# Optimization experiments

Hardware: AMD Instinct MI355X
Metric: run time of the kernel (lower is better)

Reference implementation:

```python
import jax, jax.numpy as jnp
import numpy as np

N = 100000
IN_DIM = 128
OUT_DIM = 128
E = 320000


def setup_inputs() -> dict:
    key = jax.random.key(0)
    ks = jax.random.split(key, 12)
    x = jax.random.normal(ks[0], (N, IN_DIM), dtype=jnp.float32)
    src0 = jax.random.randint(ks[1], (E,), 0, N)
    dst0 = jax.random.randint(ks[2], (E,), 0, N)
    src1 = jax.random.randint(ks[3], (E,), 0, N)
    dst1 = jax.random.randint(ks[4], (E,), 0, N)
    s = 1.0 / np.sqrt(IN_DIM)
    W0 = jax.random.uniform(ks[5], (IN_DIM, OUT_DIM), minval=-s, maxval=s)
    b0 = jax.random.uniform(ks[6], (OUT_DIM,), minval=-s, maxval=s)
    W1 = jax.random.uniform(ks[7], (IN_DIM, OUT_DIM), minval=-s, maxval=s)
    b1 = jax.random.uniform(ks[8], (OUT_DIM,), minval=-s, maxval=s)
    sa = 1.0 / np.sqrt(2 * OUT_DIM)
    a0 = jax.random.uniform(ks[9], (2 * OUT_DIM,), minval=-sa, maxval=sa)
    a1 = jax.random.uniform(ks[10], (2 * OUT_DIM,), minval=-sa, maxval=sa)
    return {"x": x, "src0": src0, "dst0": dst0, "src1": src1, "dst1": dst1,
            "W0": W0, "b0": b0, "a0": a0, "W1": W1, "b1": b1, "a1": a1}


def _rel_gat(x, src, dst, W, b, a):
    # wh = Linear(in_dim, out_dim)(x)  -> [N, D]
    wh = x @ W + b
    D = wh.shape[1]
    # e = leaky_relu(a^T [wh_src || wh_dst]) ; split a instead of concat on edges
    e = jax.nn.leaky_relu(wh[src] @ a[:D] + wh[dst] @ a[D:])  # [E]
    # segment softmax over incoming edges of each dst node
    m = jax.ops.segment_max(e, dst, num_segments=N)
    ex = jnp.exp(e - m[dst])
    denom = jax.ops.segment_sum(ex, dst, num_segments=N)
    alpha = ex / denom[dst]  # [E]
    # weighted scatter-sum of src features (zero for isolated dst nodes)
    return jax.ops.segment_sum(alpha[:, None] * wh[src], dst, num_segments=N)


def reference(x, src0, dst0, src1, dst1, W0, b0, a0, W1, b1, a1):
    h0 = _rel_gat(x, src0, dst0, W0, b0, a0)
    h1 = _rel_gat(x, src1, dst1, W1, b1, a1)
    # cross-relation 'sum' reducer
    return h0 + h1
```

## Files before the change

### kernel.cpp

```cpp
#include <hip/hip_runtime.h>
#include <hip/hip_bf16.h>


typedef __bf16 bf16x8 __attribute__((ext_vector_type(8)));
typedef float f32x4 __attribute__((ext_vector_type(4)));

#define DIM 128

__global__ __launch_bounds__(256) void gemm_wh_kernel(
    const float* __restrict__ x,
    const float* __restrict__ W0, const float* __restrict__ W1,
    const float* __restrict__ b0, const float* __restrict__ b1,
    const float* __restrict__ a0, const float* __restrict__ a1,
    const int* __restrict__ dst0, const int* __restrict__ dst1,
    unsigned* __restrict__ deg,
    __bf16* __restrict__ wh, float* __restrict__ s_src,
    float* __restrict__ s_dst, int N, int E)
{
    __shared__ __align__(16) __bf16 lW[2 * 128 * 136];
    const int tid = threadIdx.x;

    {
        const int gid = blockIdx.x * 256 + tid;
        if (gid < E) {
            atomicAdd(deg + dst0[gid], 1u);
            atomicAdd(deg + N + dst1[gid], 1u);
        }
    }

    for (int i = tid; i < 2 * 128 * 128; i += 256) {
        const int r = i >> 14, idx = i & 16383;
        const int k = idx >> 7, n = idx & 127;
        const float* W = r ? W1 : W0;
        lW[r * 17408 + n * 136 + k] = (__bf16)W[idx];
    }
    __syncthreads();

    const int lane = tid & 63;
    const int wave = tid >> 6;
    const int quad = lane >> 4;
    const int mr   = lane & 15;

    const long row0 = (long)blockIdx.x * 64 + wave * 16;
    long arow = row0 + mr;
    if (arow >= N) arow = N - 1;
    const f32x4* xr = (const f32x4*)(x + arow * DIM);

    f32x4 zero = {0.f, 0.f, 0.f, 0.f};
    f32x4 acc[2][8];
#pragma unroll
    for (int r = 0; r < 2; ++r)
#pragma unroll
        for (int t = 0; t < 8; ++t) acc[r][t] = zero;

#pragma unroll
    for (int ko = 0; ko < 128; ko += 32) {
        const int jb = (ko >> 2) + quad * 2;
        f32x4 lo = xr[jb], hi = xr[jb + 1];
        bf16x8 afrag = { (__bf16)lo.x, (__bf16)lo.y, (__bf16)lo.z, (__bf16)lo.w,
                         (__bf16)hi.x, (__bf16)hi.y, (__bf16)hi.z, (__bf16)hi.w };
#pragma unroll
        for (int r = 0; r < 2; ++r)
#pragma unroll
            for (int ct = 0; ct < 8; ++ct) {
                bf16x8 bfrag = *(const bf16x8*)(&lW[r * 17408 + (ct * 16 + mr) * 136 + ko + quad * 8]);
                acc[r][ct] = __builtin_amdgcn_mfma_f32_16x16x32_bf16(afrag, bfrag, acc[r][ct], 0, 0, 0);
            }
    }
    __syncthreads();

    __bf16* Cst = lW;
#pragma unroll
    for (int r = 0; r < 2; ++r) {
        const float* bias = r ? b1 : b0;
        const float* a    = r ? a1 : a0;
        float psr[4] = {0.f, 0.f, 0.f, 0.f};
        float pdr[4] = {0.f, 0.f, 0.f, 0.f};
#pragma unroll
        for (int ct = 0; ct < 8; ++ct) {
            const int c = ct * 16 + mr;
            const float bn = bias[c];
            const float asc = a[c], adc = a[DIM + c];
#pragma unroll
            for (int rr = 0; rr < 4; ++rr) {
                const float wv = acc[r][ct][rr] + bn;
                Cst[(wave * 16 + quad * 4 + rr) * 136 + c] = (__bf16)wv;
                psr[rr] += asc * wv;
                pdr[rr] += adc * wv;
            }
        }
#pragma unroll
        for (int off = 1; off < 16; off <<= 1) {
#pragma unroll
            for (int rr = 0; rr < 4; ++rr) {
                psr[rr] += __shfl_xor(psr[rr], off);
                pdr[rr] += __shfl_xor(pdr[rr], off);
            }
        }
        if (mr == 0) {
#pragma unroll
            for (int rr = 0; rr < 4; ++rr) {
                const long orow = row0 + quad * 4 + rr;
                if (orow < N) {
                    s_src[(size_t)r * N + orow] = psr[rr];
                    s_dst[(size_t)r * N + orow] = pdr[rr];
                }
            }
        }
        __syncthreads();
#pragma unroll
        for (int i = 0; i < 4; ++i) {
            const int chunk = tid + 256 * i;
            const int row = chunk >> 4, c8 = chunk & 15;
            bf16x8 v = *(const bf16x8*)&Cst[row * 136 + c8 * 8];
            const long grow = (long)blockIdx.x * 64 + row;
            if (grow < N)
                *(bf16x8*)(wh + ((size_t)r * N + grow) * DIM + c8 * 8) = v;
        }
        __syncthreads();
    }
}

__global__ __launch_bounds__(256) void scanA_kernel(
    const unsigned* __restrict__ deg, unsigned* __restrict__ tmp,
    unsigned* __restrict__ bsum, int n)
{
    __shared__ unsigned s[256];
    const int t = threadIdx.x;
    const int i = blockIdx.x * 256 + t;
    unsigned v = (i < n) ? deg[i] : 0u;
    s[t] = v;
    __syncthreads();
#pragma unroll
    for (int off = 1; off < 256; off <<= 1) {
        unsigned add = (t >= off) ? s[t - off] : 0u;
        __syncthreads();
        s[t] += add;
        __syncthreads();
    }
    if (i < n) tmp[i] = s[t] - v;
    if (t == 255) bsum[blockIdx.x] = s[t];
}

__global__ __launch_bounds__(256) void scanB_kernel(
    const unsigned* __restrict__ bsum, unsigned* __restrict__ bsumEx, int nb)
{
    __shared__ unsigned s[256];
    const int t = threadIdx.x;
    unsigned loc[4], sum = 0u;
#pragma unroll
    for (int k = 0; k < 4; ++k) {
        int idx = t * 4 + k;
        loc[k] = (idx < nb) ? bsum[idx] : 0u;
        sum += loc[k];
    }
    s[t] = sum;
    __syncthreads();
#pragma unroll
    for (int off = 1; off < 256; off <<= 1) {
        unsigned add = (t >= off) ? s[t - off] : 0u;
        __syncthreads();
        s[t] += add;
        __syncthreads();
    }
    unsigned run = s[t] - sum;
#pragma unroll
    for (int k = 0; k < 4; ++k) {
        int idx = t * 4 + k;
        if (idx < nb) bsumEx[idx] = run;
        run += loc[k];
    }
}

__global__ __launch_bounds__(256) void scanC_kernel(
    const unsigned* __restrict__ tmp, const unsigned* __restrict__ bsumEx,
    const unsigned* __restrict__ deg, unsigned* __restrict__ rowptr,
    unsigned* __restrict__ cursor, int n)
{
    const int i = blockIdx.x * 256 + threadIdx.x;
    if (i >= n) return;
    unsigned val = tmp[i] + bsumEx[blockIdx.x];
    rowptr[i] = val;
    cursor[i] = val;
    if (i == n - 1) rowptr[n] = val + deg[i];
}

__global__ __launch_bounds__(256) void fill_kernel(
    const int* __restrict__ src0, const int* __restrict__ dst0,
    const int* __restrict__ src1, const int* __restrict__ dst1,
    unsigned* __restrict__ cursor, unsigned* __restrict__ sorted_src,
    int N, int E)
{
    int i = blockIdx.x * 256 + threadIdx.x;
    if (i >= E) return;
    unsigned p0 = atomicAdd(cursor + dst0[i], 1u);
    sorted_src[p0] = (unsigned)src0[i];
    unsigned p1 = atomicAdd(cursor + N + dst1[i], 1u);
    sorted_src[p1] = (unsigned)src1[i];
}

__global__ __launch_bounds__(256) void aggregate_kernel(
    const unsigned* __restrict__ rowptr, const unsigned* __restrict__ sorted_src,
    const float* __restrict__ s_src, const float* __restrict__ s_dst,
    const __bf16* __restrict__ wh, float* __restrict__ out, int N)
{
    const int tid  = threadIdx.x;
    const int lane = tid & 63;
    const int sub  = lane >> 4;
    const int mr   = lane & 15;
    const int d    = blockIdx.x * 4 + (tid >> 6);
    if (d >= N) return;

    float o[8];
#pragma unroll
    for (int k = 0; k < 8; ++k) o[k] = 0.f;

#pragma unroll
    for (int r = 0; r < 2; ++r) {
        const int base = r * N + d;
        const unsigned beg = rowptr[base], end = rowptr[base + 1];
        if (beg == end) continue;
        const float sd = s_dst[base];
        const float* ss = s_src + (size_t)r * N;
        const __bf16* whr = wh + (size_t)r * N * DIM;

        float l = 0.f, a[8];
#pragma unroll
        for (int k = 0; k < 8; ++k) a[k] = 0.f;

        for (unsigned j0 = beg; j0 < end; j0 += 4) {
            const unsigned j = j0 + sub;
            const bool ok = j < end;
            const unsigned s = ok ? sorted_src[j] : 0u;
            float v = ss[s] + sd;
            v = v > 0.f ? v : 0.01f * v;
            const float e = ok ? __expf(v) : 0.f;
            bf16x8 w = *(const bf16x8*)(whr + (size_t)s * DIM + mr * 8);
            l += e;
#pragma unroll
            for (int k = 0; k < 8; ++k) a[k] += e * (float)w[k];
        }
        l += __shfl_xor(l, 16); l += __shfl_xor(l, 32);
#pragma unroll
        for (int k = 0; k < 8; ++k) {
            a[k] += __shfl_xor(a[k], 16);
            a[k] += __shfl_xor(a[k], 32);
        }
        const float inv = 1.f / l;
#pragma unroll
        for (int k = 0; k < 8; ++k) o[k] += a[k] * inv;
    }

    if (sub == 0) {
        float4 v0 = {o[0], o[1], o[2], o[3]};
        float4 v1 = {o[4], o[5], o[6], o[7]};
        float* op = out + (size_t)d * DIM + mr * 8;
        *(float4*)op       = v0;
        *(float4*)(op + 4) = v1;
    }
}

extern "C" void kernel_launch(void* const* d_in, const int* in_sizes, int n_in,
                              void* d_out, int out_size, void* d_ws, size_t ws_size,
                              hipStream_t stream) {
    const float* x = (const float*)d_in[0];
    const int* srcs[2] = {(const int*)d_in[1], (const int*)d_in[3]};
    const int* dsts[2] = {(const int*)d_in[2], (const int*)d_in[4]};
    const float* Ws[2] = {(const float*)d_in[5], (const float*)d_in[8]};
    const float* Bs[2] = {(const float*)d_in[6], (const float*)d_in[9]};
    const float* As[2] = {(const float*)d_in[7], (const float*)d_in[10]};

    const int N = in_sizes[0] / DIM;
    const int E = in_sizes[1];
    const int n2 = 2 * N;
    const int nb = (n2 + 255) / 256;
    float* out = (float*)d_out;

    char* p = (char*)d_ws;
    __bf16*   wh     = (__bf16*)p;   p += (size_t)n2 * DIM * 2;
    float*    s_src  = (float*)p;    p += (size_t)n2 * 4;
    float*    s_dst  = (float*)p;    p += (size_t)n2 * 4;
    unsigned* deg    = (unsigned*)p; p += (size_t)n2 * 4;
    unsigned* tmp    = (unsigned*)p; p += (size_t)n2 * 4;
    unsigned* rowptr = (unsigned*)p; p += (size_t)(n2 + 1) * 4;
    unsigned* cursor = (unsigned*)p; p += (size_t)n2 * 4;
    unsigned* ssrc   = (unsigned*)p; p += (size_t)2 * E * 4;
    unsigned* bsum   = (unsigned*)p; p += (size_t)nb * 4;
    unsigned* bsumEx = (unsigned*)p; p += (size_t)nb * 4;

    hipMemsetAsync(deg, 0, (size_t)n2 * 4, stream);

    const int gblocks = (N + 63) / 64;
    gemm_wh_kernel<<<gblocks, 256, 0, stream>>>(
        x, Ws[0], Ws[1], Bs[0], Bs[1], As[0], As[1],
        dsts[0], dsts[1], deg, wh, s_src, s_dst, N, E);

    scanA_kernel<<<nb, 256, 0, stream>>>(deg, tmp, bsum, n2);
    scanB_kernel<<<1, 256, 0, stream>>>(bsum, bsumEx, nb);
    scanC_kernel<<<nb, 256, 0, stream>>>(tmp, bsumEx, deg, rowptr, cursor, n2);
    fill_kernel<<<(E + 255) / 256, 256, 0, stream>>>(
        srcs[0], dsts[0], srcs[1], dsts[1], cursor, ssrc, N, E);
    aggregate_kernel<<<(N + 3) / 4, 256, 0, stream>>>(
        rowptr, ssrc, s_src, s_dst, wh, out, N);
}
```

Measured before the change: 273.9 us.

## Pre-swizzle W into MFMA fragment layout and merge scan passes

A small prep kernel converts both weight matrices to bf16 once, in the exact per-lane MFMA B-fragment order. The GEMM blocks then read fragments straight from global/L2 instead of each block converting and transposing 64 KB of W into LDS. This removes a large per-block prologue and cuts LDS to a small staging tile, which may raise occupancy. The scan block-sum pass and the offset-add pass are merged into one kernel that each block recomputes redundantly, removing one launch. The trade-off is extra global fragment loads inside the MFMA loop.

New measurement: 262.0 us. 1.05x faster.

```diff
diff --git a/kernel.cpp b/kernel.cpp
--- a/kernel.cpp
+++ b/kernel.cpp
@@ -7,9 +7,27 @@
 
 #define DIM 128
 
+__global__ __launch_bounds__(256) void prep_w_kernel(
+    const float* __restrict__ W0, const float* __restrict__ W1,
+    __bf16* __restrict__ wtf)
+{
+    const int e = blockIdx.x * 256 + threadIdx.x;
+    if (e >= 4096) return;
+    const int lane = e & 63;
+    const int ko4  = (e >> 6) & 3;
+    const int ct   = (e >> 8) & 7;
+    const int rel  = e >> 11;
+    const float* W = rel ? W1 : W0;
+    const int n  = ct * 16 + (lane & 15);
+    const int k0 = ko4 * 32 + (lane >> 4) * 8;
+    bf16x8 v;
+#pragma unroll
+    for (int j = 0; j < 8; ++j) v[j] = (__bf16)W[(k0 + j) * DIM + n];
+    *(bf16x8*)(wtf + (size_t)e * 8) = v;
+}
+
 __global__ __launch_bounds__(256) void gemm_wh_kernel(
-    const float* __restrict__ x,
-    const float* __restrict__ W0, const float* __restrict__ W1,
+    const float* __restrict__ x, const __bf16* __restrict__ wtf,
     const float* __restrict__ b0, const float* __restrict__ b1,
     const float* __restrict__ a0, const float* __restrict__ a1,
     const int* __restrict__ dst0, const int* __restrict__ dst1,
@@ -17,7 +35,7 @@
     __bf16* __restrict__ wh, float* __restrict__ s_src,
     float* __restrict__ s_dst, int N, int E)
 {
-    __shared__ __align__(16) __bf16 lW[2 * 128 * 136];
+    __shared__ __align__(16) __bf16 Cst[64 * 136];
     const int tid = threadIdx.x;
 
     {
@@ -28,14 +46,6 @@
         }
     }
 
-    for (int i = tid; i < 2 * 128 * 128; i += 256) {
-        const int r = i >> 14, idx = i & 16383;
-        const int k = idx >> 7, n = idx & 127;
-        const float* W = r ? W1 : W0;
-        lW[r * 17408 + n * 136 + k] = (__bf16)W[idx];
-    }
-    __syncthreads();
-
     const int lane = tid & 63;
     const int wave = tid >> 6;
     const int quad = lane >> 4;
@@ -46,34 +56,34 @@
     if (arow >= N) arow = N - 1;
     const f32x4* xr = (const f32x4*)(x + arow * DIM);
 
-    f32x4 zero = {0.f, 0.f, 0.f, 0.f};
-    f32x4 acc[2][8];
-#pragma unroll
-    for (int r = 0; r < 2; ++r)
-#pragma unroll
-        for (int t = 0; t < 8; ++t) acc[r][t] = zero;
-
-#pragma unroll
-    for (int ko = 0; ko < 128; ko += 32) {
-        const int jb = (ko >> 2) + quad * 2;
-        f32x4 lo = xr[jb], hi = xr[jb + 1];
-        bf16x8 afrag = { (__bf16)lo.x, (__bf16)lo.y, (__bf16)lo.z, (__bf16)lo.w,
-                         (__bf16)hi.x, (__bf16)hi.y, (__bf16)hi.z, (__bf16)hi.w };
-#pragma unroll
-        for (int r = 0; r < 2; ++r)
+    bf16x8 afrag[4];
+#pragma unroll
+    for (int ko4 = 0; ko4 < 4; ++ko4) {
+        f32x4 lo = xr[ko4 * 8 + quad * 2], hi = xr[ko4 * 8 + quad * 2 + 1];
+        afrag[ko4] = (bf16x8){ (__bf16)lo.x, (__bf16)lo.y, (__bf16)lo.z, (__bf16)lo.w,
+                               (__bf16)hi.x, (__bf16)hi.y, (__bf16)hi.z, (__bf16)hi.w };
+    }
+
+    const bf16x8* wt = (const bf16x8*)wtf;
+
+#pragma unroll
+    for (int rel = 0; rel < 2; ++rel) {
+        f32x4 zero = {0.f, 0.f, 0.f, 0.f};
+        f32x4 acc[8];
+#pragma unroll
+        for (int t = 0; t < 8; ++t) acc[t] = zero;
+
+#pragma unroll
+        for (int ko4 = 0; ko4 < 4; ++ko4) {
 #pragma unroll
             for (int ct = 0; ct < 8; ++ct) {
-                bf16x8 bfrag = *(const bf16x8*)(&lW[r * 17408 + (ct * 16 + mr) * 136 + ko + quad * 8]);
-                acc[r][ct] = __builtin_amdgcn_mfma_f32_16x16x32_bf16(afrag, bfrag, acc[r][ct], 0, 0, 0);
+                bf16x8 bfrag = wt[((rel * 8 + ct) * 4 + ko4) * 64 + lane];
+                acc[ct] = __builtin_amdgcn_mfma_f32_16x16x32_bf16(afrag[ko4], bfrag, acc[ct], 0, 0, 0);
             }
-    }
-    __syncthreads();
-
-    __bf16* Cst = lW;
-#pragma unroll
-    for (int r = 0; r < 2; ++r) {
-        const float* bias = r ? b1 : b0;
-        const float* a    = r ? a1 : a0;
+        }
+
+        const float* bias = rel ? b1 : b0;
+        const float* a    = rel ? a1 : a0;
         float psr[4] = {0.f, 0.f, 0.f, 0.f};
         float pdr[4] = {0.f, 0.f, 0.f, 0.f};
 #pragma unroll
@@ -83,7 +93,7 @@
             const float asc = a[c], adc = a[DIM + c];
 #pragma unroll
             for (int rr = 0; rr < 4; ++rr) {
-                const float wv = acc[r][ct][rr] + bn;
+                const float wv = acc[ct][rr] + bn;
                 Cst[(wave * 16 + quad * 4 + rr) * 136 + c] = (__bf16)wv;
                 psr[rr] += asc * wv;
                 pdr[rr] += adc * wv;
@@ -102,8 +112,8 @@
             for (int rr = 0; rr < 4; ++rr) {
                 const long orow = row0 + quad * 4 + rr;
                 if (orow < N) {
-                    s_src[(size_t)r * N + orow] = psr[rr];
-                    s_dst[(size_t)r * N + orow] = pdr[rr];
+                    s_src[(size_t)rel * N + orow] = psr[rr];
+                    s_dst[(size_t)rel * N + orow] = pdr[rr];
                 }
             }
         }
@@ -115,7 +125,7 @@
             bf16x8 v = *(const bf16x8*)&Cst[row * 136 + c8 * 8];
             const long grow = (long)blockIdx.x * 64 + row;
             if (grow < N)
-                *(bf16x8*)(wh + ((size_t)r * N + grow) * DIM + c8 * 8) = v;
+                *(bf16x8*)(wh + ((size_t)rel * N + grow) * DIM + c8 * 8) = v;
         }
         __syncthreads();
     }
@@ -142,10 +152,13 @@
     if (t == 255) bsum[blockIdx.x] = s[t];
 }
 
-__global__ __launch_bounds__(256) void scanB_kernel(
-    const unsigned* __restrict__ bsum, unsigned* __restrict__ bsumEx, int nb)
+__global__ __launch_bounds__(256) void scan2_kernel(
+    const unsigned* __restrict__ tmp, const unsigned* __restrict__ bsum,
+    const unsigned* __restrict__ deg, unsigned* __restrict__ rowptr,
+    unsigned* __restrict__ cursor, int n, int nb)
 {
     __shared__ unsigned s[256];
+    __shared__ unsigned ex[1024];
     const int t = threadIdx.x;
     unsigned loc[4], sum = 0u;
 #pragma unroll
@@ -166,23 +179,18 @@
     unsigned run = s[t] - sum;
 #pragma unroll
     for (int k = 0; k < 4; ++k) {
-        int idx = t * 4 + k;
-        if (idx < nb) bsumEx[idx] = run;
+        ex[t * 4 + k] = run;
         run += loc[k];
     }
-}
-
-__global__ __launch_bounds__(256) void scanC_kernel(
-    const unsigned* __restrict__ tmp, const unsigned* __restrict__ bsumEx,
-    const unsigned* __restrict__ deg, unsigned* __restrict__ rowptr,
-    unsigned* __restrict__ cursor, int n)
-{
-    const int i = blockIdx.x * 256 + threadIdx.x;
-    if (i >= n) return;
-    unsigned val = tmp[i] + bsumEx[blockIdx.x];
-    rowptr[i] = val;
-    cursor[i] = val;
-    if (i == n - 1) rowptr[n] = val + deg[i];
+    __syncthreads();
+    const unsigned pref = ex[blockIdx.x];
+    const int i = blockIdx.x * 256 + t;
+    if (i < n) {
+        unsigned val = tmp[i] + pref;
+        rowptr[i] = val;
+        cursor[i] = val;
+        if (i == n - 1) rowptr[n] = val + deg[i];
+    }
 }
 
 __global__ __launch_bounds__(256) void fill_kernel(
@@ -278,6 +286,7 @@
 
     char* p = (char*)d_ws;
     __bf16*   wh     = (__bf16*)p;   p += (size_t)n2 * DIM * 2;
+    __bf16*   wtf    = (__bf16*)p;   p += (size_t)4096 * 8 * 2;
     float*    s_src  = (float*)p;    p += (size_t)n2 * 4;
     float*    s_dst  = (float*)p;    p += (size_t)n2 * 4;
     unsigned* deg    = (unsigned*)p; p += (size_t)n2 * 4;
@@ -286,18 +295,16 @@
     unsigned* cursor = (unsigned*)p; p += (size_t)n2 * 4;
     unsigned* ssrc   = (unsigned*)p; p += (size_t)2 * E * 4;
     unsigned* bsum   = (unsigned*)p; p += (size_t)nb * 4;
-    unsigned* bsumEx = (unsigned*)p; p += (size_t)nb * 4;
 
     hipMemsetAsync(deg, 0, (size_t)n2 * 4, stream);
-
-    const int gblocks = (N + 63) / 64;
-    gemm_wh_kernel<<<gblocks, 256, 0, stream>>>(
-        x, Ws[0], Ws[1], Bs[0], Bs[1], As[0], As[1],
+    prep_w_kernel<<<16, 256, 0, stream>>>(Ws[0], Ws[1], wtf);
+
+    gemm_wh_kernel<<<(N + 63) / 64, 256, 0, stream>>>(
+        x, wtf, Bs[0], Bs[1], As[0], As[1],
         dsts[0], dsts[1], deg, wh, s_src, s_dst, N, E);
 
     scanA_kernel<<<nb, 256, 0, stream>>>(deg, tmp, bsum, n2);
-    scanB_kernel<<<1, 256, 0, stream>>>(bsum, bsumEx, nb);
-    scanC_kernel<<<nb, 256, 0, stream>>>(tmp, bsumEx, deg, rowptr, cursor, n2);
+    scan2_kernel<<<nb, 256, 0, stream>>>(tmp, bsum, deg, rowptr, cursor, n2, nb);
     fill_kernel<<<(E + 255) / 256, 256, 0, stream>>>(
         srcs[0], dsts[0], srcs[1], dsts[1], cursor, ssrc, N, E);
     aggregate_kernel<<<(N + 3) / 4, 256, 0, stream>>>(
```
